# Kernel optimization log

Hardware: AMD Instinct MI355X
Metric: run time of the kernel (lower is better)

Reference implementation:

```python
import jax, jax.numpy as jnp
import numpy as np

B = 256          # batch
S = 128 * 128    # s = imwidth*imheight (flattened image)
R = 16           # TT rank
N = 6            # number of TT cores


def setup_inputs() -> dict:
    key = jax.random.key(0)
    ks = jax.random.split(key, N + 1)
    # layeroptions['normalize']: cores divided by sqrt(sqrt(s))
    scale = 0.02 / np.sqrt(np.sqrt(S))
    ranklist = [1] + [R] * (N - 1) + [1]
    inp = {"z": jax.random.normal(ks[0], (B, S), dtype=jnp.float32)}
    for n in range(N):
        inp[f"core{n}"] = (
            jax.random.normal(ks[n + 1], (ranklist[n], S, ranklist[n + 1]), dtype=jnp.float32)
            * scale
        )
    inp["b"] = B
    return inp


def reference(z, core0, core1, core2, core3, core4, core5, b):
    # cores[k] has shape (d1, S, d2) with ranklist = [1, R, ..., R, 1]
    cores = [core0, core1, core2, core3, core4, core5]
    # f starts as TT[0][0] : (S, R)  (first core has d1 == 1)
    f = core0[0]
    # V_k[b] = sum_s z[b, s] * cores[k][:, s, :]   -> (b, d1, d2)
    # (equivalent to matmul(z, TT[k].permute(1,0,2).reshape(S, d1*d2)))
    V1 = jnp.einsum('bs,dse->bde', z, cores[1])          # (B, R, R)
    f = jnp.einsum('sd,bde->bse', f, V1)                 # (B, S, R)
    for k in range(2, N):
        Vk = jnp.einsum('bs,dse->bde', z, cores[k])      # (B, R, d2)
        f = jnp.einsum('bsd,bde->bse', f, Vk)            # (B, S, d2)
    # final d2 == 1 -> (B, S, 1) -> flatten like f.reshape(-1)
    return f.reshape(-1)
```

## Files before the change

### kernel.cpp

```cpp
#include <hip/hip_runtime.h>
#include <cstddef>
#include <cstdint>

namespace {
constexpr int kB = 256;
constexpr int kS = 16384;
constexpr int kNCol = 1040;
constexpr int kSB = kS / 8;
}

using short8 = __attribute__((ext_vector_type(8))) short;
using f32x4  = __attribute__((ext_vector_type(4))) float;

__device__ __forceinline__ unsigned short bf16_rne(float x) {
    const uint32_t u = __float_as_uint(x);
    return (unsigned short)((u + 0x7FFFu + ((u >> 16) & 1u)) >> 16);
}

__global__ __launch_bounds__(256) void fttv_split(
    const float* __restrict__ z,
    unsigned short* __restrict__ zh, unsigned short* __restrict__ zl)
{
    const int i = blockIdx.x * 256 + threadIdx.x;
    const int lr = i & 15;
    const int sblk = (i >> 4) & (kSB - 1);
    const int rowblk = i >> 15;
    const int row = rowblk * 16 + lr;
    const float* src = z + (size_t)row * kS + sblk * 8;
    float x[8];
    *reinterpret_cast<float4*>(&x[0]) = *reinterpret_cast<const float4*>(src);
    *reinterpret_cast<float4*>(&x[4]) = *reinterpret_cast<const float4*>(src + 4);
    short8 h, l;
    #pragma unroll
    for (int j = 0; j < 8; ++j) {
        const unsigned short hb = bf16_rne(x[j]);
        h[j] = (short)hb;
        const float r = x[j] - __uint_as_float((uint32_t)hb << 16);
        l[j] = (short)(__float_as_uint(r) >> 16);
    }
    const size_t idx = (((size_t)rowblk * kSB + sblk) * 16 + lr) * 8;
    *reinterpret_cast<short8*>(zh + idx) = h;
    *reinterpret_cast<short8*>(zl + idx) = l;
}

__device__ __forceinline__ void load_a(
    const unsigned short* __restrict__ zhp, const unsigned short* __restrict__ zlp,
    int sblk0, short8 ah[4], short8 al[4])
{
    #pragma unroll
    for (int fm = 0; fm < 4; ++fm) {
        const size_t o = ((size_t)fm * kSB + sblk0) * 128;
        ah[fm] = *reinterpret_cast<const short8*>(zhp + o);
        al[fm] = *reinterpret_cast<const short8*>(zlp + o);
    }
}

__device__ __forceinline__ void load_b(const float* const bptr[4], int s0,
                                       float rb[4][8])
{
    #pragma unroll
    for (int fn = 0; fn < 4; ++fn)
        #pragma unroll
        for (int j = 0; j < 8; ++j)
            rb[fn][j] = bptr[fn][(size_t)(s0 + j) * 16];
}

__device__ __forceinline__ void step_mfma(
    const short8 ah[4], const short8 al[4], const float rb[4][8],
    f32x4 acc[4][4])
{
    short8 bh[4];
    #pragma unroll
    for (int fn = 0; fn < 4; ++fn)
        #pragma unroll
        for (int j = 0; j < 8; ++j)
            bh[fn][j] = (short)bf16_rne(rb[fn][j]);
    __builtin_amdgcn_s_setprio(1);
    #pragma unroll
    for (int fn = 0; fn < 4; ++fn)
        #pragma unroll
        for (int fm = 0; fm < 4; ++fm) {
            acc[fm][fn] = __builtin_amdgcn_mfma_f32_16x16x32_bf16(
                ah[fm], bh[fn], acc[fm][fn], 0, 0, 0);
            acc[fm][fn] = __builtin_amdgcn_mfma_f32_16x16x32_bf16(
                al[fm], bh[fn], acc[fm][fn], 0, 0, 0);
        }
    __builtin_amdgcn_s_setprio(0);
}

__global__ __launch_bounds__(64, 2) void fttv_gemm_t(
    const unsigned short* __restrict__ zh, const unsigned short* __restrict__ zl,
    const float* __restrict__ c1, const float* __restrict__ c2,
    const float* __restrict__ c3, const float* __restrict__ c4,
    const float* __restrict__ c5,
    float* __restrict__ v, int kc)
{
    const int nwg = gridDim.x;
    const int q = nwg >> 3, r = nwg & 7;
    const int xcd = blockIdx.x & 7, rest = blockIdx.x >> 3;
    const int vfl = (xcd < r ? xcd * (q + 1) : r * (q + 1) + (xcd - r) * q) + rest;
    const int sk = vfl / 68;
    const int rem = vfl - sk * 68;
    const int mt = rem / 17;
    const int cg = rem - mt * 17;

    const int l = threadIdx.x;
    const int lr = l & 15, lkq = l >> 4;
    const int nsteps = kc >> 5;
    const int sb00 = sk * (kc >> 3);
    const int s0base = sk * kc + lkq * 8;

    const unsigned short* zhp = zh + ((size_t)(mt * 4) * kSB + lkq) * 128 + lr * 8;
    const unsigned short* zlp = zl + ((size_t)(mt * 4) * kSB + lkq) * 128 + lr * 8;

    f32x4 acc[4][4];
    #pragma unroll
    for (int i = 0; i < 4; ++i)
        #pragma unroll
        for (int j = 0; j < 4; ++j) acc[i][j] = (f32x4){0.f, 0.f, 0.f, 0.f};

    short8 ah0[4], al0[4], ah1[4], al1[4];

    if (cg < 16) {
        const int ci = cg >> 2;
        const float* cp = (ci == 0 ? c1 : ci == 1 ? c2 : ci == 2 ? c3 : c4);
        const int d0 = (cg & 3) * 4;
        const float* bptr[4];
        #pragma unroll
        for (int fn = 0; fn < 4; ++fn)
            bptr[fn] = cp + (size_t)(d0 + fn) * kS * 16 + lr;

        float rb0[4][8], rb1[4][8];
        load_b(bptr, s0base, rb0);
        load_a(zhp, zlp, sb00, ah0, al0);
        for (int t = 0; t < nsteps; t += 2) {
            load_b(bptr, s0base + (t + 1) * 32, rb1);
            load_a(zhp, zlp, sb00 + (t + 1) * 4, ah1, al1);
            step_mfma(ah0, al0, rb0, acc);
            if (t + 2 < nsteps) {
                load_b(bptr, s0base + (t + 2) * 32, rb0);
                load_a(zhp, zlp, sb00 + (t + 2) * 4, ah0, al0);
            }
            step_mfma(ah1, al1, rb1, acc);
        }
        #pragma unroll
        for (int fm = 0; fm < 4; ++fm)
            #pragma unroll
            for (int fn = 0; fn < 4; ++fn) {
                const int col = cg * 64 + fn * 16 + lr;
                const int brow = mt * 64 + fm * 16 + lkq * 4;
                #pragma unroll
                for (int qq = 0; qq < 4; ++qq)
                    atomicAdd(&v[(size_t)(brow + qq) * kNCol + col],
                              acc[fm][fn][qq]);
            }
    } else {
        const float* bp5 = c5 + (size_t)lr * kS;
        float r50[8], r51[8];
        load_a(zhp, zlp, sb00, ah0, al0);
        *reinterpret_cast<float4*>(&r50[0]) =
            *reinterpret_cast<const float4*>(bp5 + s0base);
        *reinterpret_cast<float4*>(&r50[4]) =
            *reinterpret_cast<const float4*>(bp5 + s0base + 4);
        for (int t = 0; t < nsteps; t += 2) {
            load_a(zhp, zlp, sb00 + (t + 1) * 4, ah1, al1);
            *reinterpret_cast<float4*>(&r51[0]) =
                *reinterpret_cast<const float4*>(bp5 + s0base + (t + 1) * 32);
            *reinterpret_cast<float4*>(&r51[4]) =
                *reinterpret_cast<const float4*>(bp5 + s0base + (t + 1) * 32 + 4);
            {
                short8 bh;
                #pragma unroll
                for (int j = 0; j < 8; ++j) bh[j] = (short)bf16_rne(r50[j]);
                #pragma unroll
                for (int fm = 0; fm < 4; ++fm) {
                    acc[fm][0] = __builtin_amdgcn_mfma_f32_16x16x32_bf16(
                        ah0[fm], bh, acc[fm][0], 0, 0, 0);
                    acc[fm][0] = __builtin_amdgcn_mfma_f32_16x16x32_bf16(
                        al0[fm], bh, acc[fm][0], 0, 0, 0);
                }
            }
            if (t + 2 < nsteps) {
                load_a(zhp, zlp, sb00 + (t + 2) * 4, ah0, al0);
                *reinterpret_cast<float4*>(&r50[0]) =
                    *reinterpret_cast<const float4*>(bp5 + s0base + (t + 2) * 32);
                *reinterpret_cast<float4*>(&r50[4]) =
                    *reinterpret_cast<const float4*>(bp5 + s0base + (t + 2) * 32 + 4);
            }
            {
                short8 bh;
                #pragma unroll
                for (int j = 0; j < 8; ++j) bh[j] = (short)bf16_rne(r51[j]);
                #pragma unroll
                for (int fm = 0; fm < 4; ++fm) {
                    acc[fm][0] = __builtin_amdgcn_mfma_f32_16x16x32_bf16(
                        ah1[fm], bh, acc[fm][0], 0, 0, 0);
                    acc[fm][0] = __builtin_amdgcn_mfma_f32_16x16x32_bf16(
                        al1[fm], bh, acc[fm][0], 0, 0, 0);
                }
            }
        }
        #pragma unroll
        for (int fm = 0; fm < 4; ++fm) {
            const int col = 1024 + lr;
            const int brow = mt * 64 + fm * 16 + lkq * 4;
            #pragma unroll
            for (int qq = 0; qq < 4; ++qq)
                atomicAdd(&v[(size_t)(brow + qq) * kNCol + col], acc[fm][0][qq]);
        }
    }
}

__global__ void fttv_chain(const float* __restrict__ v, float* __restrict__ w)
{
    const int b = blockIdx.x;
    const float* vb = v + (size_t)b * kNCol;
    const int lane = threadIdx.x;
    const int d = lane & 15;
    float u = vb[1024 + d];
    #pragma unroll
    for (int k = 4; k >= 1; --k) {
        float nu = 0.f;
        #pragma unroll
        for (int e = 0; e < 16; ++e) {
            const float ue = __shfl(u, e, 16);
            nu += vb[(k - 1) * 256 + d * 16 + e] * ue;
        }
        u = nu;
    }
    if (lane < 16) w[b * 16 + d] = u;
}

__global__ __launch_bounds__(256) void fttv_out(
    const float* __restrict__ c0, const float* __restrict__ w,
    float* __restrict__ out)
{
    __shared__ float wl[64][16];
    const int sc = blockIdx.x & 63;
    const int bq = blockIdx.x >> 6;
    const int tid = threadIdx.x;
    const int s = sc * 256 + tid;
    float f0[16];
    #pragma unroll
    for (int q = 0; q < 4; ++q)
        *reinterpret_cast<float4*>(&f0[q * 4]) =
            *reinterpret_cast<const float4*>(c0 + (size_t)s * 16 + q * 4);
    *reinterpret_cast<float4*>(&wl[0][0] + tid * 4) =
        *reinterpret_cast<const float4*>(w + bq * 1024 + tid * 4);
    __syncthreads();
    for (int bb = 0; bb < 64; ++bb) {
        float a = 0.f;
        #pragma unroll
        for (int d = 0; d < 16; ++d) a += f0[d] * wl[bb][d];
        out[(size_t)(bq * 64 + bb) * kS + s] = a;
    }
}

extern "C" void kernel_launch(void* const* d_in, const int* in_sizes, int n_in,
                              void* d_out, int out_size, void* d_ws, size_t ws_size,
                              hipStream_t stream)
{
    (void)in_sizes; (void)n_in; (void)out_size; (void)ws_size;
    const float* z  = (const float*)d_in[0];
    const float* c0 = (const float*)d_in[1];
    const float* c1 = (const float*)d_in[2];
    const float* c2 = (const float*)d_in[3];
    const float* c3 = (const float*)d_in[4];
    const float* c4 = (const float*)d_in[5];
    const float* c5 = (const float*)d_in[6];
    float* out = (float*)d_out;
    float* ws  = (float*)d_ws;

    const size_t zhlF = (size_t)kB * kS;
    const int splitk = 32;
    const int kc = kS / splitk;

    unsigned short* zh = (unsigned short*)ws;
    unsigned short* zl = zh + (size_t)kB * kS;
    float* v = ws + zhlF;
    float* w = v + (size_t)kNCol * kB;

    hipMemsetAsync(v, 0, (size_t)kNCol * kB * sizeof(float), stream);
    fttv_split<<<dim3((kB * kS / 8) / 256), 256, 0, stream>>>(z, zh, zl);
    fttv_gemm_t<<<dim3(68 * splitk), 64, 0, stream>>>(
        zh, zl, c1, c2, c3, c4, c5, v, kc);
    fttv_chain<<<dim3(kB), 64, 0, stream>>>(v, w);
    fttv_out<<<dim3(256), 256, 0, stream>>>(c0, w, out);
}
```

Measured before the change: 85.12 us.

## Pre-convert TT cores to bf16 MFMA-fragment layout in a separate kernel

Adds a kernel that converts cores 1-5 to bf16 once and stores them in the blocked fragment layout the MFMA operands expect. The GEMM kernel then loads B fragments as contiguous short8 vectors instead of strided fp32 gathers with per-step conversion, and its prefetch schedule now keeps two steps of A and B in flight. Each core is converted once rather than once per batch tile, and the strided gather of up to 32 scalars per lane per step is removed. The cost is an extra kernel launch plus a write and re-read of roughly 34 MB of bf16 B data through workspace.

```diff
diff --git a/kernel.cpp b/kernel.cpp
--- a/kernel.cpp
+++ b/kernel.cpp
@@ -43,6 +43,34 @@
     *reinterpret_cast<short8*>(zl + idx) = l;
 }
 
+__global__ __launch_bounds__(256) void fttv_bconv(
+    const float* __restrict__ c1, const float* __restrict__ c2,
+    const float* __restrict__ c3, const float* __restrict__ c4,
+    const float* __restrict__ c5, unsigned short* __restrict__ bbf)
+{
+    const int i = blockIdx.x * 256 + threadIdx.x;
+    const int lc = i & 15;
+    const int sblk = (i >> 4) & (kSB - 1);
+    const int cblk = i >> 15;
+    float x[8];
+    if (cblk < 64) {
+        const float* cp = (cblk < 16 ? c1 : cblk < 32 ? c2 : cblk < 48 ? c3 : c4);
+        const int d = cblk & 15;
+        const float* src = cp + ((size_t)d * kS + sblk * 8) * 16 + lc;
+        #pragma unroll
+        for (int j = 0; j < 8; ++j) x[j] = src[(size_t)j * 16];
+    } else {
+        const float* src = c5 + (size_t)lc * kS + sblk * 8;
+        *reinterpret_cast<float4*>(&x[0]) = *reinterpret_cast<const float4*>(src);
+        *reinterpret_cast<float4*>(&x[4]) = *reinterpret_cast<const float4*>(src + 4);
+    }
+    short8 h;
+    #pragma unroll
+    for (int j = 0; j < 8; ++j) h[j] = (short)bf16_rne(x[j]);
+    *reinterpret_cast<short8*>(
+        bbf + (((size_t)cblk * kSB + sblk) * 16 + lc) * 8) = h;
+}
+
 __device__ __forceinline__ void load_a(
     const unsigned short* __restrict__ zhp, const unsigned short* __restrict__ zlp,
     int sblk0, short8 ah[4], short8 al[4])
@@ -55,29 +83,24 @@
     }
 }
 
-__device__ __forceinline__ void load_b(const float* const bptr[4], int s0,
-                                       float rb[4][8])
-{
-    #pragma unroll
-    for (int fn = 0; fn < 4; ++fn)
-        #pragma unroll
-        for (int j = 0; j < 8; ++j)
-            rb[fn][j] = bptr[fn][(size_t)(s0 + j) * 16];
-}
-
+template <int NFN>
+__device__ __forceinline__ void load_bt(
+    const unsigned short* __restrict__ bp, int sblk0, short8 bh[NFN])
+{
+    #pragma unroll
+    for (int fn = 0; fn < NFN; ++fn)
+        bh[fn] = *reinterpret_cast<const short8*>(
+            bp + ((size_t)fn * kSB + sblk0) * 128);
+}
+
+template <int NFN>
 __device__ __forceinline__ void step_mfma(
-    const short8 ah[4], const short8 al[4], const float rb[4][8],
+    const short8 ah[4], const short8 al[4], const short8 bh[NFN],
     f32x4 acc[4][4])
 {
-    short8 bh[4];
-    #pragma unroll
-    for (int fn = 0; fn < 4; ++fn)
-        #pragma unroll
-        for (int j = 0; j < 8; ++j)
-            bh[fn][j] = (short)bf16_rne(rb[fn][j]);
     __builtin_amdgcn_s_setprio(1);
     #pragma unroll
-    for (int fn = 0; fn < 4; ++fn)
+    for (int fn = 0; fn < NFN; ++fn)
         #pragma unroll
         for (int fm = 0; fm < 4; ++fm) {
             acc[fm][fn] = __builtin_amdgcn_mfma_f32_16x16x32_bf16(
@@ -90,9 +113,7 @@
 
 __global__ __launch_bounds__(64, 2) void fttv_gemm_t(
     const unsigned short* __restrict__ zh, const unsigned short* __restrict__ zl,
-    const float* __restrict__ c1, const float* __restrict__ c2,
-    const float* __restrict__ c3, const float* __restrict__ c4,
-    const float* __restrict__ c5,
+    const unsigned short* __restrict__ bbf,
     float* __restrict__ v, int kc)
 {
     const int nwg = gridDim.x;
@@ -107,11 +128,11 @@
     const int l = threadIdx.x;
     const int lr = l & 15, lkq = l >> 4;
     const int nsteps = kc >> 5;
-    const int sb00 = sk * (kc >> 3);
-    const int s0base = sk * kc + lkq * 8;
-
-    const unsigned short* zhp = zh + ((size_t)(mt * 4) * kSB + lkq) * 128 + lr * 8;
-    const unsigned short* zlp = zl + ((size_t)(mt * 4) * kSB + lkq) * 128 + lr * 8;
+    const int sb0 = sk * (kc >> 3) + lkq;
+
+    const unsigned short* zhp = zh + (size_t)(mt * 4) * kSB * 128 + lr * 8;
+    const unsigned short* zlp = zl + (size_t)(mt * 4) * kSB * 128 + lr * 8;
+    const unsigned short* bp  = bbf + (size_t)(cg * 4) * kSB * 128 + lr * 8;
 
     f32x4 acc[4][4];
     #pragma unroll
@@ -122,26 +143,22 @@
     short8 ah0[4], al0[4], ah1[4], al1[4];
 
     if (cg < 16) {
-        const int ci = cg >> 2;
-        const float* cp = (ci == 0 ? c1 : ci == 1 ? c2 : ci == 2 ? c3 : c4);
-        const int d0 = (cg & 3) * 4;
-        const float* bptr[4];
-        #pragma unroll
-        for (int fn = 0; fn < 4; ++fn)
-            bptr[fn] = cp + (size_t)(d0 + fn) * kS * 16 + lr;
-
-        float rb0[4][8], rb1[4][8];
-        load_b(bptr, s0base, rb0);
-        load_a(zhp, zlp, sb00, ah0, al0);
+        short8 bh0[4], bh1[4];
+        load_bt<4>(bp, sb0, bh0);
+        load_a(zhp, zlp, sb0, ah0, al0);
+        load_bt<4>(bp, sb0 + 4, bh1);
+        load_a(zhp, zlp, sb0 + 4, ah1, al1);
         for (int t = 0; t < nsteps; t += 2) {
-            load_b(bptr, s0base + (t + 1) * 32, rb1);
-            load_a(zhp, zlp, sb00 + (t + 1) * 4, ah1, al1);
-            step_mfma(ah0, al0, rb0, acc);
+            step_mfma<4>(ah0, al0, bh0, acc);
             if (t + 2 < nsteps) {
-                load_b(bptr, s0base + (t + 2) * 32, rb0);
-                load_a(zhp, zlp, sb00 + (t + 2) * 4, ah0, al0);
-            }
-            step_mfma(ah1, al1, rb1, acc);
+                load_bt<4>(bp, sb0 + (t + 2) * 4, bh0);
+                load_a(zhp, zlp, sb0 + (t + 2) * 4, ah0, al0);
+            }
+            step_mfma<4>(ah1, al1, bh1, acc);
+            if (t + 3 < nsteps) {
+                load_bt<4>(bp, sb0 + (t + 3) * 4, bh1);
+                load_a(zhp, zlp, sb0 + (t + 3) * 4, ah1, al1);
+            }
         }
         #pragma unroll
         for (int fm = 0; fm < 4; ++fm)
@@ -155,49 +172,21 @@
                               acc[fm][fn][qq]);
             }
     } else {
-        const float* bp5 = c5 + (size_t)lr * kS;
-        float r50[8], r51[8];
-        load_a(zhp, zlp, sb00, ah0, al0);
-        *reinterpret_cast<float4*>(&r50[0]) =
-            *reinterpret_cast<const float4*>(bp5 + s0base);
-        *reinterpret_cast<float4*>(&r50[4]) =
-            *reinterpret_cast<const float4*>(bp5 + s0base + 4);
+        short8 bh0[1], bh1[1];
+        load_bt<1>(bp, sb0, bh0);
+        load_a(zhp, zlp, sb0, ah0, al0);
+        load_bt<1>(bp, sb0 + 4, bh1);
+        load_a(zhp, zlp, sb0 + 4, ah1, al1);
         for (int t = 0; t < nsteps; t += 2) {
-            load_a(zhp, zlp, sb00 + (t + 1) * 4, ah1, al1);
-            *reinterpret_cast<float4*>(&r51[0]) =
-                *reinterpret_cast<const float4*>(bp5 + s0base + (t + 1) * 32);
-            *reinterpret_cast<float4*>(&r51[4]) =
-                *reinterpret_cast<const float4*>(bp5 + s0base + (t + 1) * 32 + 4);
-            {
-                short8 bh;
-                #pragma unroll
-                for (int j = 0; j < 8; ++j) bh[j] = (short)bf16_rne(r50[j]);
-                #pragma unroll
-                for (int fm = 0; fm < 4; ++fm) {
-                    acc[fm][0] = __builtin_amdgcn_mfma_f32_16x16x32_bf16(
-                        ah0[fm], bh, acc[fm][0], 0, 0, 0);
-                    acc[fm][0] = __builtin_amdgcn_mfma_f32_16x16x32_bf16(
-                        al0[fm], bh, acc[fm][0], 0, 0, 0);
-                }
-            }
+            step_mfma<1>(ah0, al0, bh0, acc);
             if (t + 2 < nsteps) {
-                load_a(zhp, zlp, sb00 + (t + 2) * 4, ah0, al0);
-                *reinterpret_cast<float4*>(&r50[0]) =
-                    *reinterpret_cast<const float4*>(bp5 + s0base + (t + 2) * 32);
-                *reinterpret_cast<float4*>(&r50[4]) =
-                    *reinterpret_cast<const float4*>(bp5 + s0base + (t + 2) * 32 + 4);
-            }
-            {
-                short8 bh;
-                #pragma unroll
-                for (int j = 0; j < 8; ++j) bh[j] = (short)bf16_rne(r51[j]);
-                #pragma unroll
-                for (int fm = 0; fm < 4; ++fm) {
-                    acc[fm][0] = __builtin_amdgcn_mfma_f32_16x16x32_bf16(
-                        ah1[fm], bh, acc[fm][0], 0, 0, 0);
-                    acc[fm][0] = __builtin_amdgcn_mfma_f32_16x16x32_bf16(
-                        al1[fm], bh, acc[fm][0], 0, 0, 0);
-                }
+                load_bt<1>(bp, sb0 + (t + 2) * 4, bh0);
+                load_a(zhp, zlp, sb0 + (t + 2) * 4, ah0, al0);
+            }
+            step_mfma<1>(ah1, al1, bh1, acc);
+            if (t + 3 < nsteps) {
+                load_bt<1>(bp, sb0 + (t + 3) * 4, bh1);
+                load_a(zhp, zlp, sb0 + (t + 3) * 4, ah1, al1);
             }
         }
         #pragma unroll
@@ -272,18 +261,21 @@
     float* ws  = (float*)d_ws;
 
     const size_t zhlF = (size_t)kB * kS;
+    const size_t bbfF = (size_t)kNCol * kS / 2;
     const int splitk = 32;
     const int kc = kS / splitk;
 
     unsigned short* zh = (unsigned short*)ws;
     unsigned short* zl = zh + (size_t)kB * kS;
-    float* v = ws + zhlF;
+    unsigned short* bbf = (unsigned short*)(ws + zhlF);
+    float* v = ws + zhlF + bbfF;
     float* w = v + (size_t)kNCol * kB;
 
     hipMemsetAsync(v, 0, (size_t)kNCol * kB * sizeof(float), stream);
     fttv_split<<<dim3((kB * kS / 8) / 256), 256, 0, stream>>>(z, zh, zl);
-    fttv_gemm_t<<<dim3(68 * splitk), 64, 0, stream>>>(
-        zh, zl, c1, c2, c3, c4, c5, v, kc);
+    fttv_bconv<<<dim3(65 * kSB * 16 / 256), 256, 0, stream>>>(
+        c1, c2, c3, c4, c5, bbf);
+    fttv_gemm_t<<<dim3(68 * splitk), 64, 0, stream>>>(zh, zl, bbf, v, kc);
     fttv_chain<<<dim3(kB), 64, 0, stream>>>(v, w);
     fttv_out<<<dim3(256), 256, 0, stream>>>(c0, w, out);
 }
```

After: 91.25 us. 7.2% more time.
